# Optimization experiments

Hardware: AMD Instinct MI355X
Metric: run time of the kernel (lower is better)

## Reference

```python
import jax, jax.numpy as jnp
import numpy as np

B, T, N, H, E, K, HOR, OD = 64, 12, 1024, 64, 16, 3, 12, 1
DIN = 1  # input_dim
EPS = 1e-12


def setup_inputs() -> dict:
    key = jax.random.key(0)
    ks = jax.random.split(key, 8)
    s = 0.02
    return {
        "source": jax.random.normal(ks[0], (B, T, N, DIN), jnp.float32),
        "node_emb": jax.random.normal(ks[1], (N, E), jnp.float32),
        "time_emb": jax.random.normal(ks[2], (T, E), jnp.float32),
        "gate_wp": jax.random.normal(ks[3], (E, K, DIN + H, 2 * H), jnp.float32) * s,
        "gate_bp": jax.random.normal(ks[4], (E, 2 * H), jnp.float32) * s,
        "gate_lng": jnp.ones((E,), jnp.float32),
        "gate_lnb": jnp.zeros((E,), jnp.float32),
        "upd_wp": jax.random.normal(ks[5], (E, K, DIN + H, H), jnp.float32) * s,
        "upd_bp": jax.random.normal(ks[6], (E, H), jnp.float32) * s,
        "upd_lng": jnp.ones((E,), jnp.float32),
        "upd_lnb": jnp.zeros((E,), jnp.float32),
        "out_lng": jnp.ones((H,), jnp.float32),
        "out_lnb": jnp.zeros((H,), jnp.float32),
        "conv_w": jax.random.normal(ks[7], (HOR * OD, H), jnp.float32) * s,
        "conv_b": jnp.zeros((HOR * OD,), jnp.float32),
    }


def _ln(x, g, b):
    m = x.mean(-1, keepdims=True)
    v = x.var(-1, keepdims=True)
    return (x - m) / jnp.sqrt(v + EPS) * g + b


def _dagcn(x, node_emb, t_emb, wp, bp, lng, lnb):
    # x: [B, N, C]; node_emb: [N, E]; t_emb: [E] (one timestep)
    e = _ln(node_emb + t_emb[None, :], lng, lnb)          # [N, E] (dropout off in eval)
    sup = jax.nn.softmax(e @ e.T, axis=1)                  # [N, N]
    sl = [jnp.eye(N, dtype=x.dtype), sup]
    for _ in range(2, K):
        sl.append(2.0 * sup @ sl[-1] - sl[-2])             # Chebyshev recursion
    S = jnp.stack(sl, axis=0)                              # [K, N, N]
    w = jnp.einsum('nd,dkio->nkio', e, wp)                 # per-node weights
    bias = e @ bp                                          # [N, O]
    xg = jnp.einsum('knm,bmc->bnkc', S, x)                 # graph conv
    return jnp.einsum('bnki,nkio->bno', xg, w) + bias


def reference(source, node_emb, time_emb, gate_wp, gate_bp, gate_lng, gate_lnb,
              upd_wp, upd_bp, upd_lng, upd_lnb, out_lng, out_lnb, conv_w, conv_b):
    def step(state, xs):
        x_t, te = xs                                        # [B,N,DIN], [E]
        zr = jax.nn.sigmoid(_dagcn(jnp.concatenate([x_t, state], -1),
                                   node_emb, te, gate_wp, gate_bp, gate_lng, gate_lnb))
        z, r = zr[..., :H], zr[..., H:]
        hc = jnp.tanh(_dagcn(jnp.concatenate([x_t, z * state], -1),
                             node_emb, te, upd_wp, upd_bp, upd_lng, upd_lnb))
        h = r * state + (1.0 - r) * hc
        return h, None

    xs = jnp.swapaxes(source, 0, 1)                        # [T,B,N,DIN]
    h0 = jnp.zeros((B, N, H), source.dtype)
    h, _ = jax.lax.scan(step, h0, (xs, time_emb))          # last hidden state [B,N,H]
    y = _ln(h, out_lng, out_lnb)                           # out_dropout off in eval
    out = jnp.einsum('bnh,oh->bon', y, conv_w) + conv_b[None, :, None]  # end_conv
    return out.reshape(B, HOR, OD, N).transpose(0, 1, 3, 2)  # [B,horizon,N,output_dim]
```

## Files before the change

### kernel.cpp

```cpp
#include <hip/hip_runtime.h>
#include <math.h>

namespace {
constexpr int B_ = 64, T_ = 12, N_ = 1024, H_ = 64, E_ = 16;
constexpr int C_  = 65;
constexpr int BC_ = B_ * C_;
constexpr int NPAD_ = 4224;
constexpr int OG_ = 128;
constexpr int OU_ = 64;
constexpr float EPS_ = 1e-12f;
constexpr int KP_ = 224;
constexpr int KS_ = 232;
constexpr int COLG_ = OG_ * KP_;
constexpr int COLU_ = OU_ * KP_;
constexpr int NE_ = N_ * E_;
}

typedef unsigned short u16;
typedef unsigned int u32;
using f16x8 = __attribute__((ext_vector_type(8))) _Float16;
using f16x4 = __attribute__((ext_vector_type(4))) _Float16;
using f32x4 = __attribute__((ext_vector_type(4))) float;

__device__ __forceinline__ u32 div65(u32 x) { return (x * 16135u) >> 20; }
__device__ __forceinline__ u32 div29(u32 x) { return (x * 565u) >> 14; }

__device__ __forceinline__ void gl_lds16(const void* g, void* l, int lane) {
#if __has_builtin(__builtin_amdgcn_global_load_lds)
  __builtin_amdgcn_global_load_lds((const __attribute__((address_space(1))) u32*)g,
                                   (__attribute__((address_space(3))) u32*)l, 16, 0, 0);
#else
  *(uint4*)((char*)l + lane * 16) = *(const uint4*)g;
#endif
}

__device__ __forceinline__ void wprep_body(const float* __restrict__ wp, int NO,
                                           _Float16* __restrict__ wpC, int k, int tid) {
  if (tid >= NO) return;
  f16x8 lo = {}, hi = {};
  if (k < 195) {
    const u32 seg = div65((u32)k);
    const u32 ii = k - seg * 65;
#pragma unroll
    for (int d = 0; d < 8; d++)
      lo[d] = (_Float16)wp[(((size_t)d * 3 + seg) * 65 + ii) * NO + tid];
#pragma unroll
    for (int d = 0; d < 8; d++)
      hi[d] = (_Float16)wp[(((size_t)(d + 8) * 3 + seg) * 65 + ii) * NO + tid];
  }
  _Float16* dst = &wpC[((size_t)tid * KP_ + k) * 16];
  *(f16x8*)dst = lo;
  *(f16x8*)(dst + 8) = hi;
}

__device__ __forceinline__ void sup_body(const float* __restrict__ eT,
                                         _Float16* __restrict__ s16,
                                         int n, int tid, float* red) {
  float en[E_];
#pragma unroll
  for (int d = 0; d < E_; d++) en[d] = eT[d * N_ + n];
  float lg[4];
  float mx = -3.4e38f;
#pragma unroll
  for (int j = 0; j < 4; j++) {
    int m = tid + 256 * j;
    float s = 0.f;
#pragma unroll
    for (int d = 0; d < E_; d++) s = fmaf(en[d], eT[d * N_ + m], s);
    lg[j] = s;
    mx = fmaxf(mx, s);
  }
  red[tid] = mx; __syncthreads();
  for (int off = 128; off > 0; off >>= 1) {
    if (tid < off) red[tid] = fmaxf(red[tid], red[tid + off]);
    __syncthreads();
  }
  mx = red[0]; __syncthreads();
  float sum = 0.f;
#pragma unroll
  for (int j = 0; j < 4; j++) { lg[j] = __expf(lg[j] - mx); sum += lg[j]; }
  red[tid] = sum; __syncthreads();
  for (int off = 128; off > 0; off >>= 1) {
    if (tid < off) red[tid] += red[tid + off];
    __syncthreads();
  }
  float inv = 1.0f / red[0];
#pragma unroll
  for (int j = 0; j < 4; j++)
    s16[(size_t)n * N_ + tid + 256 * j] = (_Float16)(lg[j] * inv);
}

__device__ __forceinline__ void wgen_body(const float* __restrict__ e,
                                          const _Float16* __restrict__ wpC, int COLS,
                                          _Float16* __restrict__ Wt,
                                          int xb, int yb, int tid, float (*es)[16]) {
  const int col0 = xb * 1024 + tid * 4;
  const int n0 = yb * 64;
#pragma unroll
  for (int q = 0; q < 4; q++) {
    int idx = tid + q * 256;
    es[idx >> 4][idx & 15] = e[(size_t)n0 * 16 + idx];
  }
  __syncthreads();
  float wc[4][16];
#pragma unroll
  for (int cc = 0; cc < 4; cc++) {
    f16x8 a = *(const f16x8*)&wpC[(size_t)(col0 + cc) * 16];
    f16x8 b = *(const f16x8*)&wpC[(size_t)(col0 + cc) * 16 + 8];
#pragma unroll
    for (int d = 0; d < 8; d++) { wc[cc][d] = (float)a[d]; wc[cc][8 + d] = (float)b[d]; }
  }
  for (int nn = 0; nn < 64; nn++) {
    float acc[4] = {};
#pragma unroll
    for (int d = 0; d < 16; d++) {
      float ev = es[nn][d];
#pragma unroll
      for (int cc = 0; cc < 4; cc++) acc[cc] = fmaf(ev, wc[cc][d], acc[cc]);
    }
    f16x4 pv;
#pragma unroll
    for (int cc = 0; cc < 4; cc++) pv[cc] = (_Float16)acc[cc];
    *(f16x4*)&Wt[(size_t)(n0 + nn) * COLS + col0] = pv;
  }
}

__device__ __forceinline__ void supT_body(const _Float16* __restrict__ S,
                                          _Float16* __restrict__ ST,
                                          int tile, int tid, _Float16 (*lds)[66]) {
  const int n0 = (tile >> 4) * 64;
  const int m0 = (tile & 15) * 64;
  {
    const int r = tid >> 2, c0 = (tid & 3) * 16;
    const _Float16* sp = &S[(size_t)(n0 + r) * 1024 + m0 + c0];
    f16x8 a = *(const f16x8*)sp;
    f16x8 b = *(const f16x8*)(sp + 8);
#pragma unroll
    for (int i = 0; i < 8; i++) { lds[r][c0 + i] = a[i]; lds[r][c0 + 8 + i] = b[i]; }
  }
  __syncthreads();
  {
    const int c = tid >> 2, r0 = (tid & 3) * 16;
    f16x8 a, b;
#pragma unroll
    for (int i = 0; i < 8; i++) { a[i] = lds[r0 + i][c]; b[i] = lds[r0 + 8 + i][c]; }
    _Float16* dp = &ST[(size_t)(m0 + c) * 1024 + n0 + r0];
    *(f16x8*)dp = a;
    *(f16x8*)(dp + 8) = b;
  }
}

__device__ __forceinline__ void gemm_body(
    const _Float16* __restrict__ A, const _Float16* __restrict__ Bt,
    _Float16* __restrict__ rowout,
    int bx, int by, int tid, _Float16* As, _Float16* Bs) {
  const int wave = tid >> 6, lane = tid & 63;
  const int m0 = by * 128, c0 = bx * 64;
  const int lrow = lane >> 3;
  const int lchunk = lane & 7;
  const int fm = lane & 15, fq = lane >> 4;
  f32x4 acc[2][4] = {};
  for (int ks = 0; ks < 16; ks++) {
    const int kp = ks * 64;
#pragma unroll
    for (int q = 0; q < 4; q++) {
      const int seg = wave * 4 + q;
      const int row = seg * 8 + lrow;
      const int sw = lchunk ^ (row & 7);
      gl_lds16(A + (size_t)(m0 + row) * 1024 + kp + sw * 8, &As[seg * 8 * 64], lane);
    }
#pragma unroll
    for (int q = 0; q < 2; q++) {
      const int seg = wave * 2 + q;
      const int row = seg * 8 + lrow;
      const int sw = lchunk ^ (row & 7);
      gl_lds16(Bt + (size_t)(c0 + row) * 1024 + kp + sw * 8, &Bs[seg * 8 * 64], lane);
    }
    __syncthreads();
#pragma unroll
    for (int kk = 0; kk < 2; kk++) {
      f16x8 af[2], bfr[4];
      const int g = kk * 4 + fq;
#pragma unroll
      for (int mt = 0; mt < 2; mt++) {
        const int row = wave * 32 + mt * 16 + fm;
        af[mt] = *(const f16x8*)&As[row * 64 + (g ^ (row & 7)) * 8];
      }
#pragma unroll
      for (int nt = 0; nt < 4; nt++) {
        const int row = nt * 16 + fm;
        bfr[nt] = *(const f16x8*)&Bs[row * 64 + (g ^ (row & 7)) * 8];
      }
#pragma unroll
      for (int mt = 0; mt < 2; mt++)
#pragma unroll
        for (int nt = 0; nt < 4; nt++)
          acc[mt][nt] = __builtin_amdgcn_mfma_f32_16x16x32_f16(af[mt], bfr[nt], acc[mt][nt], 0, 0, 0);
    }
    __syncthreads();
  }
  const int q4 = fq * 4;
#pragma unroll
  for (int nt = 0; nt < 4; nt++) {
    const int col = c0 + nt * 16 + fm;
#pragma unroll
    for (int mt = 0; mt < 2; mt++) {
      const int row = m0 + wave * 32 + mt * 16 + q4;
      const f32x4 v = acc[mt][nt];
#pragma unroll
      for (int j = 0; j < 4; j++)
        rowout[(size_t)(row + j) * 1024 + col] = (_Float16)v[j];
    }
  }
}

__device__ __forceinline__ void gemm2_body(
    const _Float16* __restrict__ A1, const _Float16* __restrict__ A2,
    const _Float16* __restrict__ Bt,
    _Float16* __restrict__ y1row, _Float16* __restrict__ y2row,
    int bx, int by, int tid,
    _Float16* As1, _Float16* As2, _Float16* Bs) {
  const int wave = tid >> 6, lane = tid & 63;
  const int m0 = by * 128, c0 = bx * 64;
  const int lrow = lane >> 3;
  const int lchunk = lane & 7;
  const int fm = lane & 15, fq = lane >> 4;
  f32x4 acc1[2][4] = {}, acc2[2][4] = {};
  for (int ks = 0; ks < 16; ks++) {
    const int kp = ks * 64;
#pragma unroll
    for (int q = 0; q < 4; q++) {
      const int seg = wave * 4 + q;
      const int row = seg * 8 + lrow;
      const int sw = lchunk ^ (row & 7);
      const size_t go = (size_t)(m0 + row) * 1024 + kp + sw * 8;
      gl_lds16(A1 + go, &As1[seg * 8 * 64], lane);
      gl_lds16(A2 + go, &As2[seg * 8 * 64], lane);
    }
#pragma unroll
    for (int q = 0; q < 2; q++) {
      const int seg = wave * 2 + q;
      const int row = seg * 8 + lrow;
      const int sw = lchunk ^ (row & 7);
      gl_lds16(Bt + (size_t)(c0 + row) * 1024 + kp + sw * 8, &Bs[seg * 8 * 64], lane);
    }
    __syncthreads();
#pragma unroll
    for (int kk = 0; kk < 2; kk++) {
      f16x8 a1[2], a2[2], bfr[4];
      const int g = kk * 4 + fq;
#pragma unroll
      for (int mt = 0; mt < 2; mt++) {
        const int row = wave * 32 + mt * 16 + fm;
        const int o = row * 64 + (g ^ (row & 7)) * 8;
        a1[mt] = *(const f16x8*)&As1[o];
        a2[mt] = *(const f16x8*)&As2[o];
      }
#pragma unroll
      for (int nt = 0; nt < 4; nt++) {
        const int row = nt * 16 + fm;
        bfr[nt] = *(const f16x8*)&Bs[row * 64 + (g ^ (row & 7)) * 8];
      }
#pragma unroll
      for (int mt = 0; mt < 2; mt++)
#pragma unroll
        for (int nt = 0; nt < 4; nt++) {
          acc1[mt][nt] = __builtin_amdgcn_mfma_f32_16x16x32_f16(a1[mt], bfr[nt], acc1[mt][nt], 0, 0, 0);
          acc2[mt][nt] = __builtin_amdgcn_mfma_f32_16x16x32_f16(a2[mt], bfr[nt], acc2[mt][nt], 0, 0, 0);
        }
    }
    __syncthreads();
  }
  const int q4 = fq * 4;
#pragma unroll
  for (int nt = 0; nt < 4; nt++) {
    const int col = c0 + nt * 16 + fm;
    if (col >= BC_) continue;
#pragma unroll
    for (int mt = 0; mt < 2; mt++) {
      const int row = m0 + wave * 32 + mt * 16 + q4;
      const f32x4 v1 = acc1[mt][nt];
      const f32x4 v2 = acc2[mt][nt];
#pragma unroll
      for (int j = 0; j < 4; j++) {
        y1row[(size_t)(row + j) * BC_ + col] = (_Float16)v1[j];
        y2row[(size_t)(row + j) * BC_ + col] = (_Float16)v2[j];
      }
    }
  }
}

__device__ __forceinline__ void stage_xg(
    const _Float16* __restrict__ x0p, const _Float16* __restrict__ y1p,
    const _Float16* __restrict__ y2p, int tid, _Float16* __restrict__ XGs) {
  for (int idx = tid; idx < BC_; idx += 256) {
    const u32 b = div65((u32)idx), k = (u32)idx - b * 65;
    XGs[b * KS_ + k] = x0p[idx];
  }
  for (int idx = tid; idx < BC_; idx += 256) {
    const u32 b = div65((u32)idx), k = (u32)idx - b * 65;
    XGs[b * KS_ + 65 + k] = y1p[idx];
  }
  for (int idx = tid; idx < BC_; idx += 256) {
    const u32 b = div65((u32)idx), k = (u32)idx - b * 65;
    XGs[b * KS_ + 130 + k] = (_Float16)(2.f * (float)y2p[idx] - (float)x0p[idx]);
  }
  for (int idx = tid; idx < 64 * 29; idx += 256) {
    const u32 b = div29((u32)idx), k = (u32)idx - b * 29;
    XGs[b * KS_ + 195 + k] = (_Float16)0.f;
  }
}

__global__ __launch_bounds__(256) void k_pre0(
    const float* __restrict__ gate_wp, const float* __restrict__ upd_wp,
    _Float16* __restrict__ wpCg, _Float16* __restrict__ wpCu,
    const float* __restrict__ node_emb, const float* __restrict__ time_emb,
    const float* __restrict__ g_lng, const float* __restrict__ g_lnb,
    const float* __restrict__ u_lng, const float* __restrict__ u_lnb,
    float* __restrict__ eg_all, float* __restrict__ egT_all,
    float* __restrict__ eu_all, float* __restrict__ euT_all) {
  const int bid = blockIdx.x, tid = threadIdx.x;
  if (bid < KP_)     { wprep_body(gate_wp, OG_, wpCg, bid, tid); return; }
  if (bid < 2 * KP_) { wprep_body(upd_wp,  OU_, wpCu, bid - KP_, tid); return; }
  const int idx = bid - 2 * KP_;
  const int t = idx >> 2;
  const int n = (idx & 3) * 256 + tid;
  float v[E_];
  float m = 0.f;
#pragma unroll
  for (int d = 0; d < E_; d++) { v[d] = node_emb[n * E_ + d] + time_emb[t * E_ + d]; m += v[d]; }
  m *= (1.0f / E_);
  float var = 0.f;
#pragma unroll
  for (int d = 0; d < E_; d++) { float x = v[d] - m; var += x * x; }
  var *= (1.0f / E_);
  float rs = rsqrtf(var + EPS_);
#pragma unroll
  for (int d = 0; d < E_; d++) {
    float nv = (v[d] - m) * rs;
    float g = nv * g_lng[d] + g_lnb[d];
    float u = nv * u_lng[d] + u_lnb[d];
    eg_all[(size_t)t * NE_ + n * E_ + d] = g;
    egT_all[(size_t)t * NE_ + d * N_ + n] = g;
    eu_all[(size_t)t * NE_ + n * E_ + d] = u;
    euT_all[(size_t)t * NE_ + d * N_ + n] = u;
  }
}

__global__ __launch_bounds__(256) void k_pro(
    const float* __restrict__ egT0, const float* __restrict__ euT0,
    const float* __restrict__ src,
    _Float16* __restrict__ supG, _Float16* __restrict__ supU0,
    _Float16* __restrict__ Xt, _Float16* __restrict__ X0row) {
  __shared__ float red[256];
  const int bid = blockIdx.x, tid = threadIdx.x;
  if (bid < 1024) { sup_body(egT0, supG, bid, tid, red); return; }
  if (bid < 2048) { sup_body(euT0, supU0, bid - 1024, tid, red); return; }
  const int idx = bid - 2048;
  const int b = idx & 63, m0 = (idx >> 6) * 64;
  for (int q = 0; q < 17; q++) {
    int i = tid + q * 256;
    if (i < 64 * 65) {
      int c = i >> 6, m = i & 63;
      float xv = (c == 0) ? src[((size_t)b * T_) * N_ + m0 + m] : 0.f;
      Xt[((size_t)(b * C_ + c)) * 1024 + m0 + m] = (_Float16)xv;
      u32 mm = div65((u32)i), cc = (u32)i - mm * 65;
      float xv2 = (cc == 0) ? src[((size_t)b * T_) * N_ + m0 + mm] : 0.f;
      X0row[((size_t)(m0 + mm)) * BC_ + b * 65 + cc] = (_Float16)xv2;
    }
  }
}

__global__ __launch_bounds__(256) void k_proT(
    const _Float16* __restrict__ supG0, const _Float16* __restrict__ supU0,
    _Float16* __restrict__ supGT, _Float16* __restrict__ supUT) {
  __shared__ _Float16 lds[64][66];
  const int bid = blockIdx.x;
  if (bid < 256) supT_body(supG0, supGT, bid, threadIdx.x, lds);
  else           supT_body(supU0, supUT, bid - 256, threadIdx.x, lds);
}

__global__ __launch_bounds__(256) void k_pro2(
    const _Float16* __restrict__ supG0, const _Float16* __restrict__ supGT,
    const _Float16* __restrict__ supU0, const _Float16* __restrict__ supUT,
    _Float16* __restrict__ sup2G0, _Float16* __restrict__ sup2U0) {
  __shared__ __align__(16) _Float16 smem[12288];
  const int bid = blockIdx.x, tid = threadIdx.x;
  if (bid < 128)
    gemm_body(supG0, supGT, sup2G0, bid % 16, bid / 16, tid, smem, smem + 8192);
  else
    gemm_body(supU0, supUT, sup2U0, (bid - 128) % 16, (bid - 128) / 16, tid, smem, smem + 8192);
}

__global__ __launch_bounds__(256) void k_tr(const _Float16* __restrict__ X0,
                                            _Float16* __restrict__ Xt) {
  __shared__ _Float16 tile[64][66];
  const int c0 = (blockIdx.x % 65) * 64;
  const int m0 = (blockIdx.x / 65) * 64;
  const int tid = threadIdx.x;
#pragma unroll
  for (int q = 0; q < 16; q++) {
    int idx = tid + q * 256;
    int m = idx >> 6, c = idx & 63;
    tile[m][c] = X0[(size_t)(m0 + m) * BC_ + c0 + c];
  }
  __syncthreads();
  {
    const int c = tid >> 2, mq = (tid & 3) * 16;
    f16x8 a, b;
#pragma unroll
    for (int i = 0; i < 8; i++) { a[i] = tile[mq + i][c]; b[i] = tile[mq + 8 + i][c]; }
    _Float16* dp = &Xt[(size_t)(c0 + c) * 1024 + m0 + mq];
    *(f16x8*)dp = a;
    *(f16x8*)(dp + 8) = b;
  }
}

__global__ __launch_bounds__(256) void k_ga(
    const _Float16* __restrict__ supG_t, const _Float16* __restrict__ sup2G_t,
    const _Float16* __restrict__ Xt,
    _Float16* __restrict__ y1row, _Float16* __restrict__ y2row,
    const float* __restrict__ eg_t, const _Float16* __restrict__ wpCg,
    _Float16* __restrict__ WtG,
    const float* __restrict__ egT_nx, const float* __restrict__ euT_nx,
    _Float16* __restrict__ supG_nx, _Float16* __restrict__ supU_nx) {
  __shared__ __align__(16) _Float16 smem[20480];
  const int bid = blockIdx.x, tid = threadIdx.x;
  if (bid < 528) {
    gemm2_body(supG_t, sup2G_t, Xt, y1row, y2row, bid % 66, bid / 66, tid,
               smem, smem + 8192, smem + 16384);
  } else if (bid < 976) {
    const int w = bid - 528;
    wgen_body(eg_t, wpCg, COLG_, WtG, w % 28, w / 28, tid, (float(*)[16])smem);
  } else if (bid < 2000) {
    sup_body(egT_nx, supG_nx, bid - 976, tid, (float*)smem);
  } else {
    sup_body(euT_nx, supU_nx, bid - 2000, tid, (float*)smem);
  }
}

__global__ __launch_bounds__(256) void k_cgT(
    const float* __restrict__ eg,
    const _Float16* __restrict__ X0, const _Float16* __restrict__ y1r,
    const _Float16* __restrict__ y2r,
    const _Float16* __restrict__ Wt, const float* __restrict__ bp,
    const _Float16* __restrict__ h16, const float* __restrict__ src, int t,
    _Float16* __restrict__ r16, _Float16* X0out,
    const _Float16* __restrict__ supG_nx, const _Float16* __restrict__ supU_nx,
    _Float16* __restrict__ supGT, _Float16* __restrict__ supUT) {
  __shared__ __align__(16) char smraw[30272];
  const int bid = blockIdx.x;
  const int tid = threadIdx.x;
  if (bid >= 1024) {
    _Float16 (*lds)[66] = (_Float16(*)[66])smraw;
    if (bid < 1280) supT_body(supG_nx, supGT, bid - 1024, tid, lds);
    else            supT_body(supU_nx, supUT, bid - 1280, tid, lds);
    return;
  }
  float* es = (float*)smraw;
  float* bias_s = (float*)(smraw + 64);
  _Float16* XGs = (_Float16*)(smraw + 576);
  _Float16 (*zs)[72] = (_Float16(*)[72])(smraw + 576);
  _Float16 (*rs)[72] = (_Float16(*)[72])(smraw + 9792);
  const int n = bid;
  const int wave = tid >> 6, lane = tid & 63;
  const int fm = lane & 15, fq = lane >> 4;
  const int wm = wave >> 1, wn = wave & 1;
  if (tid < 16) es[tid] = eg[n * 16 + tid];
  stage_xg(X0 + (size_t)n * BC_, y1r + (size_t)n * BC_, y2r + (size_t)n * BC_, tid, XGs);
  __syncthreads();
  if (tid < 128) {
    float bv = 0.f;
#pragma unroll
    for (int d = 0; d < 16; d++) bv = fmaf(es[d], bp[d * OG_ + tid], bv);
    bias_s[tid] = bv;
  }
  const _Float16* Bb = Wt + (size_t)n * OG_ * KP_;
  f32x4 acc[2][4] = {};
#pragma unroll
  for (int kk = 0; kk < 7; kk++) {
    const int ko = kk * 32 + fq * 8;
    f16x8 af[2], bf[4];
#pragma unroll
    for (int mt = 0; mt < 2; mt++)
      af[mt] = *(const f16x8*)&XGs[(wm * 32 + mt * 16 + fm) * KS_ + ko];
#pragma unroll
    for (int nt = 0; nt < 4; nt++)
      bf[nt] = *(const f16x8*)&Bb[(wn * 64 + nt * 16 + fm) * KP_ + ko];
#pragma unroll
    for (int mt = 0; mt < 2; mt++)
#pragma unroll
      for (int nt = 0; nt < 4; nt++)
        acc[mt][nt] = __builtin_amdgcn_mfma_f32_16x16x32_f16(af[mt], bf[nt], acc[mt][nt], 0, 0, 0);
  }
  __syncthreads();
#pragma unroll
  for (int nt = 0; nt < 4; nt++) {
    const int o = wn * 64 + nt * 16 + fm;
    const float bias = bias_s[o];
#pragma unroll
    for (int mt = 0; mt < 2; mt++) {
      const f32x4 v = acc[mt][nt];
#pragma unroll
      for (int j = 0; j < 4; j++) {
        const int b = wm * 32 + mt * 16 + fq * 4 + j;
        float s = 1.0f / (1.0f + __expf(-(v[j] + bias)));
        if (wn == 0) zs[b][o] = (_Float16)s;
        else         rs[b][o - H_] = (_Float16)s;
      }
    }
  }
  __syncthreads();
  {
    const int b = tid >> 2, q = tid & 3;
    const _Float16* hp = &h16[((size_t)b * N_ + n) * H_ + q * 16];
    _Float16* xp = &X0out[(size_t)n * BC_ + b * 65 + 1 + q * 16];
    _Float16* rp = &r16[((size_t)b * N_ + n) * H_ + q * 16];
    f16x8 r0, r1;
#pragma unroll
    for (int i = 0; i < 8; i++) {
      r0[i] = rs[b][q * 16 + i];
      r1[i] = rs[b][q * 16 + 8 + i];
    }
    *(f16x8*)rp = r0;
    *(f16x8*)(rp + 8) = r1;
    f16x8 h0 = *(const f16x8*)hp;
    f16x8 h1 = *(const f16x8*)(hp + 8);
    f16x8 x0, x1;
#pragma unroll
    for (int i = 0; i < 8; i++) {
      x0[i] = (_Float16)((float)zs[b][q * 16 + i] * (float)h0[i]);
      x1[i] = (_Float16)((float)zs[b][q * 16 + 8 + i] * (float)h1[i]);
    }
    *(f16x8*)xp = x0;
    *(f16x8*)(xp + 8) = x1;
    if (tid < 64) {
      float sv = src[((size_t)tid * T_ + t) * N_ + n];
      X0out[(size_t)n * BC_ + tid * 65] = (_Float16)sv;
    }
  }
}

__global__ __launch_bounds__(256) void k_gu(
    const _Float16* __restrict__ supU_t, const _Float16* __restrict__ sup2U_t,
    const _Float16* __restrict__ Xt,
    _Float16* __restrict__ y1row, _Float16* __restrict__ y2row,
    const float* __restrict__ eu_t, const _Float16* __restrict__ wpCu,
    _Float16* __restrict__ WtU,
    const _Float16* __restrict__ supG_nx, const _Float16* __restrict__ supGT,
    const _Float16* __restrict__ supU_nx, const _Float16* __restrict__ supUT,
    _Float16* __restrict__ sup2G_nx, _Float16* __restrict__ sup2U_nx) {
  __shared__ __align__(16) _Float16 smem[20480];
  const int bid = blockIdx.x, tid = threadIdx.x;
  if (bid < 528) {
    gemm2_body(supU_t, sup2U_t, Xt, y1row, y2row, bid % 66, bid / 66, tid,
               smem, smem + 8192, smem + 16384);
  } else if (bid < 752) {
    const int w = bid - 528;
    wgen_body(eu_t, wpCu, COLU_, WtU, w % 14, w / 14, tid, (float(*)[16])smem);
  } else if (bid < 880) {
    const int w = bid - 752;
    gemm_body(supG_nx, supGT, sup2G_nx, w % 16, w / 16, tid, smem, smem + 8192);
  } else {
    const int w = bid - 880;
    gemm_body(supU_nx, supUT, sup2U_nx, w % 16, w / 16, tid, smem, smem + 8192);
  }
}

__global__ __launch_bounds__(256) void k_cu(
    const float* __restrict__ eu,
    const _Float16* __restrict__ X0, const _Float16* __restrict__ y1r,
    const _Float16* __restrict__ y2r,
    const _Float16* __restrict__ Wt, const float* __restrict__ bp,
    const _Float16* __restrict__ r16, const float* __restrict__ src,
    int t, int donext,
    _Float16* __restrict__ h16, _Float16* X0out) {
  __shared__ __align__(16) char smraw[30016];
  float* es = (float*)smraw;
  float* bias_s = (float*)(smraw + 64);
  _Float16* XGs = (_Float16*)(smraw + 320);
  _Float16 (*hs)[72] = (_Float16(*)[72])(smraw + 320);
  _Float16 (*rs)[72] = (_Float16(*)[72])(smraw + 9536);
  const int n = blockIdx.x;
  const int tid = threadIdx.x;
  const int wave = tid >> 6, lane = tid & 63;
  const int fm = lane & 15, fq = lane >> 4;
  if (tid < 16) es[tid] = eu[n * 16 + tid];
  stage_xg(X0 + (size_t)n * BC_, y1r + (size_t)n * BC_, y2r + (size_t)n * BC_, tid, XGs);
  __syncthreads();
  if (tid < 64) {
    float bv = 0.f;
#pragma unroll
    for (int d = 0; d < 16; d++) bv = fmaf(es[d], bp[d * OU_ + tid], bv);
    bias_s[tid] = bv;
  }
  const _Float16* Bb = Wt + (size_t)n * OU_ * KP_;
  f32x4 acc[4] = {};
#pragma unroll
  for (int kk = 0; kk < 7; kk++) {
    const int ko = kk * 32 + fq * 8;
    f16x8 af = *(const f16x8*)&XGs[(wave * 16 + fm) * KS_ + ko];
    f16x8 bf[4];
#pragma unroll
    for (int nt = 0; nt < 4; nt++)
      bf[nt] = *(const f16x8*)&Bb[(nt * 16 + fm) * KP_ + ko];
#pragma unroll
    for (int nt = 0; nt < 4; nt++)
      acc[nt] = __builtin_amdgcn_mfma_f32_16x16x32_f16(af, bf[nt], acc[nt], 0, 0, 0);
  }
  __syncthreads();
  {
    const int b = tid >> 2, q = tid & 3;
    const _Float16* hp = &h16[((size_t)b * N_ + n) * H_ + q * 16];
    const _Float16* rp = &r16[((size_t)b * N_ + n) * H_ + q * 16];
    f16x8 h0 = *(const f16x8*)hp;
    f16x8 h1 = *(const f16x8*)(hp + 8);
    f16x8 r0 = *(const f16x8*)rp;
    f16x8 r1 = *(const f16x8*)(rp + 8);
#pragma unroll
    for (int i = 0; i < 8; i++) {
      hs[b][q * 16 + i] = h0[i];
      hs[b][q * 16 + 8 + i] = h1[i];
      rs[b][q * 16 + i] = r0[i];
      rs[b][q * 16 + 8 + i] = r1[i];
    }
  }
  __syncthreads();
#pragma unroll
  for (int nt = 0; nt < 4; nt++) {
    const int o = nt * 16 + fm;
    const float bias = bias_s[o];
    const f32x4 v = acc[nt];
#pragma unroll
    for (int j = 0; j < 4; j++) {
      const int b = wave * 16 + fq * 4 + j;
      float hc = tanhf(v[j] + bias);
      float rv = (float)rs[b][o];
      float hv = (float)hs[b][o];
      hs[b][o] = (_Float16)(rv * hv + (1.0f - rv) * hc);
    }
  }
  __syncthreads();
  {
    const int b = tid >> 2, q = tid & 3;
    _Float16* hp = &h16[((size_t)b * N_ + n) * H_ + q * 16];
    f16x8 h0, h1;
#pragma unroll
    for (int i = 0; i < 8; i++) {
      h0[i] = hs[b][q * 16 + i];
      h1[i] = hs[b][q * 16 + 8 + i];
    }
    *(f16x8*)hp = h0;
    *(f16x8*)(hp + 8) = h1;
    if (donext) {
      _Float16* xp = &X0out[(size_t)n * BC_ + b * 65 + 1 + q * 16];
      *(f16x8*)xp = h0;
      *(f16x8*)(xp + 8) = h1;
      if (tid < 64) {
        float sv = src[((size_t)tid * T_ + (t + 1)) * N_ + n];
        X0out[(size_t)n * BC_ + tid * 65] = (_Float16)sv;
      }
    }
  }
}

__global__ __launch_bounds__(256) void k_final(const _Float16* __restrict__ h16,
                                               const float* __restrict__ out_lng,
                                               const float* __restrict__ out_lnb,
                                               const float* __restrict__ conv_w,
                                               const float* __restrict__ conv_b,
                                               float* __restrict__ out) {
  const int b = blockIdx.x >> 2;
  const int n = (blockIdx.x & 3) * 256 + threadIdx.x;
  __shared__ float cw[12][64];
  __shared__ float cb[12];
  __shared__ float lgs[64], lbs[64];
  for (int idx = threadIdx.x; idx < 12 * 64; idx += 256) cw[idx >> 6][idx & 63] = conv_w[idx];
  if (threadIdx.x < 12) cb[threadIdx.x] = conv_b[threadIdx.x];
  if (threadIdx.x < 64) { lgs[threadIdx.x] = out_lng[threadIdx.x]; lbs[threadIdx.x] = out_lnb[threadIdx.x]; }
  __syncthreads();
  const _Float16* hp = &h16[((size_t)b * N_ + n) * H_];
  float hv[64];
  float mean = 0.f;
#pragma unroll
  for (int i8 = 0; i8 < 8; i8++) {
    f16x8 v = *(const f16x8*)&hp[i8 * 8];
#pragma unroll
    for (int j = 0; j < 8; j++) { hv[i8 * 8 + j] = (float)v[j]; mean += hv[i8 * 8 + j]; }
  }
  mean *= (1.0f / H_);
  float var = 0.f;
#pragma unroll
  for (int i = 0; i < 64; i++) { float d = hv[i] - mean; var += d * d; }
  var *= (1.0f / H_);
  const float rs = rsqrtf(var + EPS_);
  float y[64];
#pragma unroll
  for (int i = 0; i < 64; i++)
    y[i] = (hv[i] - mean) * rs * lgs[i] + lbs[i];
#pragma unroll
  for (int o = 0; o < 12; o++) {
    float acc = cb[o];
#pragma unroll
    for (int i = 0; i < 64; i++) acc = fmaf(y[i], cw[o][i], acc);
    out[((size_t)b * 12 + o) * N_ + n] = acc;
  }
}

extern "C" void kernel_launch(void* const* d_in, const int* in_sizes, int n_in,
                              void* d_out, int out_size, void* d_ws, size_t ws_size,
                              hipStream_t stream) {
  const float* src      = (const float*)d_in[0];
  const float* node_emb = (const float*)d_in[1];
  const float* time_emb = (const float*)d_in[2];
  const float* gate_wp  = (const float*)d_in[3];
  const float* gate_bp  = (const float*)d_in[4];
  const float* gate_lng = (const float*)d_in[5];
  const float* gate_lnb = (const float*)d_in[6];
  const float* upd_wp   = (const float*)d_in[7];
  const float* upd_bp   = (const float*)d_in[8];
  const float* upd_lng  = (const float*)d_in[9];
  const float* upd_lnb  = (const float*)d_in[10];
  const float* out_lng  = (const float*)d_in[11];
  const float* out_lnb  = (const float*)d_in[12];
  const float* conv_w   = (const float*)d_in[13];
  const float* conv_b   = (const float*)d_in[14];
  float* out = (float*)d_out;

  constexpr size_t SZ_H16 = (size_t)B_ * N_ * H_ / 2;
  constexpr size_t SZ_R   = SZ_H16;
  constexpr size_t SZ_T   = (size_t)NPAD_ * 1024 / 2;
  constexpr size_t SZ_ROW = (size_t)N_ * BC_ / 2;
  constexpr size_t SZ_WT  = (size_t)N_ * OG_ * KP_ / 2;
  constexpr size_t SZ_WCG = (size_t)COLG_ * 16 / 2;
  constexpr size_t SZ_WCU = (size_t)COLU_ * 16 / 2;
  constexpr size_t SZ_S   = (size_t)N_ * N_ / 2;

  float* ws = (float*)d_ws;
  size_t off = 0;
  float* h16F   = ws + off; off += SZ_H16;
  float* r16F   = ws + off; off += SZ_R;
  float* XtF    = ws + off; off += SZ_T;
  float* X0F    = ws + off; off += SZ_ROW;
  float* y1F    = ws + off; off += SZ_ROW;
  float* y2F    = ws + off; off += SZ_ROW;
  float* WtF    = ws + off; off += SZ_WT;
  float* wcgF   = ws + off; off += SZ_WCG;
  float* wcuF   = ws + off; off += SZ_WCU;
  float* supGF  = ws + off; off += 2 * SZ_S;
  float* supUF  = ws + off; off += 2 * SZ_S;
  float* supGTF = ws + off; off += SZ_S;
  float* supUTF = ws + off; off += SZ_S;
  float* s2GF   = ws + off; off += 2 * SZ_S;
  float* s2UF   = ws + off; off += 2 * SZ_S;
  float* eg_all  = ws + off; off += (size_t)T_ * NE_;
  float* egT_all = ws + off; off += (size_t)T_ * NE_;
  float* eu_all  = ws + off; off += (size_t)T_ * NE_;
  float* euT_all = ws + off; off += (size_t)T_ * NE_;
  if (ws_size < off * sizeof(float)) return;

  _Float16* h16   = (_Float16*)h16F;
  _Float16* r16   = (_Float16*)r16F;
  _Float16* Xt    = (_Float16*)XtF;
  _Float16* X0row = (_Float16*)X0F;
  _Float16* y1row = (_Float16*)y1F;
  _Float16* y2row = (_Float16*)y2F;
  _Float16* WtG   = (_Float16*)WtF;
  _Float16* WtU   = (_Float16*)WtF;
  _Float16* wpCg  = (_Float16*)wcgF;
  _Float16* wpCu  = (_Float16*)wcuF;
  _Float16* supG  = (_Float16*)supGF;
  _Float16* supU  = (_Float16*)supUF;
  _Float16* supGT = (_Float16*)supGTF;
  _Float16* supUT = (_Float16*)supUTF;
  _Float16* s2G   = (_Float16*)s2GF;
  _Float16* s2U   = (_Float16*)s2UF;
  const size_t SB = (size_t)N_ * N_;

  hipMemsetAsync(h16, 0, SZ_H16 * sizeof(float), stream);
  k_pre0<<<2 * KP_ + 48, 256, 0, stream>>>(gate_wp, upd_wp, wpCg, wpCu,
                                           node_emb, time_emb,
                                           gate_lng, gate_lnb, upd_lng, upd_lnb,
                                           eg_all, egT_all, eu_all, euT_all);
  k_pro<<<3072, 256, 0, stream>>>(egT_all, euT_all, src, supG, supU, Xt, X0row);
  k_proT<<<512, 256, 0, stream>>>(supG, supU, supGT, supUT);
  k_pro2<<<256, 256, 0, stream>>>(supG, supGT, supU, supUT, s2G, s2U);

  for (int t = 0; t < T_; t++) {
    const int cur = t & 1, nxt = (t + 1) & 1;
    _Float16* supG_t  = supG + (size_t)cur * SB;
    _Float16* supG_nx = supG + (size_t)nxt * SB;
    _Float16* supU_t  = supU + (size_t)cur * SB;
    _Float16* supU_nx = supU + (size_t)nxt * SB;
    _Float16* s2G_t   = s2G + (size_t)cur * SB;
    _Float16* s2G_nx  = s2G + (size_t)nxt * SB;
    _Float16* s2U_t   = s2U + (size_t)cur * SB;
    _Float16* s2U_nx  = s2U + (size_t)nxt * SB;
    const float* eg_t = eg_all + (size_t)t * NE_;
    const float* eu_t = eu_all + (size_t)t * NE_;
    const int more = (t < T_ - 1) ? 1 : 0;
    const int tn = more ? t + 1 : t;

    k_ga<<<more ? 3024 : 976, 256, 0, stream>>>(
        supG_t, s2G_t, Xt, y1row, y2row, eg_t, wpCg, WtG,
        egT_all + (size_t)tn * NE_, euT_all + (size_t)tn * NE_, supG_nx, supU_nx);
    k_cgT<<<more ? 1536 : 1024, 256, 0, stream>>>(
        eg_t, X0row, y1row, y2row, WtG, gate_bp, h16, src, t, r16, X0row,
        supG_nx, supU_nx, supGT, supUT);
    k_tr<<<1040, 256, 0, stream>>>(X0row, Xt);
    k_gu<<<more ? 1008 : 752, 256, 0, stream>>>(
        supU_t, s2U_t, Xt, y1row, y2row, eu_t, wpCu, WtU,
        supG_nx, supGT, supU_nx, supUT, s2G_nx, s2U_nx);
    k_cu<<<N_, 256, 0, stream>>>(eu_t, X0row, y1row, y2row, WtU, upd_bp, r16,
                                 src, t, more, h16, X0row);
    if (more) k_tr<<<1040, 256, 0, stream>>>(X0row, Xt);
  }
  k_final<<<B_ * N_ / 256, 256, 0, stream>>>(h16, out_lng, out_lnb, conv_w, conv_b, out);
}
```

Before: 1.880 ms.

## Precompute all timestep supports and Chebyshev squares upfront in batched kernels

Moves the per-timestep support softmax, transpose and sup@sup GEMM out of the recurrent loop. They are now computed for all 12 timesteps in a few large batched launches before the scan, and the in-loop kernels carry only their own work. This trades fine-grained overlap of next-step support work with current-step kernels for large, well-filled launches and smaller in-loop grids. It costs much more workspace memory: 24 support matrices, 24 squared matrices and 12 transpose buffers.

```diff
diff --git a/kernel.cpp b/kernel.cpp
--- a/kernel.cpp
+++ b/kernel.cpp
@@ -347,16 +347,26 @@
   }
 }
 
-__global__ __launch_bounds__(256) void k_pro(
-    const float* __restrict__ egT0, const float* __restrict__ euT0,
+__global__ __launch_bounds__(256) void k_supall(
+    const float* __restrict__ egT_all, const float* __restrict__ euT_all,
     const float* __restrict__ src,
-    _Float16* __restrict__ supG, _Float16* __restrict__ supU0,
+    _Float16* __restrict__ supA,
     _Float16* __restrict__ Xt, _Float16* __restrict__ X0row) {
   __shared__ float red[256];
   const int bid = blockIdx.x, tid = threadIdx.x;
-  if (bid < 1024) { sup_body(egT0, supG, bid, tid, red); return; }
-  if (bid < 2048) { sup_body(euT0, supU0, bid - 1024, tid, red); return; }
-  const int idx = bid - 2048;
+  const size_t SB = (size_t)N_ * N_;
+  if (bid < 12288) {
+    const int t = bid >> 10, n = bid & 1023;
+    sup_body(egT_all + (size_t)t * NE_, supA + (size_t)(2 * t) * SB, n, tid, red);
+    return;
+  }
+  if (bid < 24576) {
+    const int idx = bid - 12288;
+    const int t = idx >> 10, n = idx & 1023;
+    sup_body(euT_all + (size_t)t * NE_, supA + (size_t)(2 * t + 1) * SB, n, tid, red);
+    return;
+  }
+  const int idx = bid - 24576;
   const int b = idx & 63, m0 = (idx >> 6) * 64;
   for (int q = 0; q < 17; q++) {
     int i = tid + q * 256;
@@ -371,25 +381,26 @@
   }
 }
 
-__global__ __launch_bounds__(256) void k_proT(
-    const _Float16* __restrict__ supG0, const _Float16* __restrict__ supU0,
-    _Float16* __restrict__ supGT, _Float16* __restrict__ supUT) {
+__global__ __launch_bounds__(256) void k_supT_half(
+    const _Float16* __restrict__ supA, _Float16* __restrict__ supTb, int half) {
   __shared__ _Float16 lds[64][66];
-  const int bid = blockIdx.x;
-  if (bid < 256) supT_body(supG0, supGT, bid, threadIdx.x, lds);
-  else           supT_body(supU0, supUT, bid - 256, threadIdx.x, lds);
-}
-
-__global__ __launch_bounds__(256) void k_pro2(
-    const _Float16* __restrict__ supG0, const _Float16* __restrict__ supGT,
-    const _Float16* __restrict__ supU0, const _Float16* __restrict__ supUT,
-    _Float16* __restrict__ sup2G0, _Float16* __restrict__ sup2U0) {
+  const size_t SB = (size_t)N_ * N_;
+  const int tile = blockIdx.x & 255;
+  const int p = blockIdx.x >> 8;
+  const int s = 2 * (half * 6 + (p >> 1)) + (p & 1);
+  supT_body(supA + (size_t)s * SB, supTb + (size_t)p * SB, tile, threadIdx.x, lds);
+}
+
+__global__ __launch_bounds__(256) void k_sup2_half(
+    const _Float16* __restrict__ supA, const _Float16* __restrict__ supTb,
+    _Float16* __restrict__ sup2A, int half) {
   __shared__ __align__(16) _Float16 smem[12288];
-  const int bid = blockIdx.x, tid = threadIdx.x;
-  if (bid < 128)
-    gemm_body(supG0, supGT, sup2G0, bid % 16, bid / 16, tid, smem, smem + 8192);
-  else
-    gemm_body(supU0, supUT, sup2U0, (bid - 128) % 16, (bid - 128) / 16, tid, smem, smem + 8192);
+  const size_t SB = (size_t)N_ * N_;
+  const int tile = blockIdx.x & 127;
+  const int p = blockIdx.x >> 7;
+  const int s = 2 * (half * 6 + (p >> 1)) + (p & 1);
+  gemm_body(supA + (size_t)s * SB, supTb + (size_t)p * SB, sup2A + (size_t)s * SB,
+            tile % 16, tile / 16, threadIdx.x, smem, smem + 8192);
 }
 
 __global__ __launch_bounds__(256) void k_tr(const _Float16* __restrict__ X0,
@@ -421,48 +432,33 @@
     const _Float16* __restrict__ Xt,
     _Float16* __restrict__ y1row, _Float16* __restrict__ y2row,
     const float* __restrict__ eg_t, const _Float16* __restrict__ wpCg,
-    _Float16* __restrict__ WtG,
-    const float* __restrict__ egT_nx, const float* __restrict__ euT_nx,
-    _Float16* __restrict__ supG_nx, _Float16* __restrict__ supU_nx) {
+    _Float16* __restrict__ WtG) {
   __shared__ __align__(16) _Float16 smem[20480];
   const int bid = blockIdx.x, tid = threadIdx.x;
   if (bid < 528) {
     gemm2_body(supG_t, sup2G_t, Xt, y1row, y2row, bid % 66, bid / 66, tid,
                smem, smem + 8192, smem + 16384);
-  } else if (bid < 976) {
+  } else {
     const int w = bid - 528;
     wgen_body(eg_t, wpCg, COLG_, WtG, w % 28, w / 28, tid, (float(*)[16])smem);
-  } else if (bid < 2000) {
-    sup_body(egT_nx, supG_nx, bid - 976, tid, (float*)smem);
-  } else {
-    sup_body(euT_nx, supU_nx, bid - 2000, tid, (float*)smem);
-  }
-}
-
-__global__ __launch_bounds__(256) void k_cgT(
+  }
+}
+
+__global__ __launch_bounds__(256) void k_cg(
     const float* __restrict__ eg,
     const _Float16* __restrict__ X0, const _Float16* __restrict__ y1r,
     const _Float16* __restrict__ y2r,
     const _Float16* __restrict__ Wt, const float* __restrict__ bp,
     const _Float16* __restrict__ h16, const float* __restrict__ src, int t,
-    _Float16* __restrict__ r16, _Float16* X0out,
-    const _Float16* __restrict__ supG_nx, const _Float16* __restrict__ supU_nx,
-    _Float16* __restrict__ supGT, _Float16* __restrict__ supUT) {
+    _Float16* __restrict__ r16, _Float16* X0out) {
   __shared__ __align__(16) char smraw[30272];
-  const int bid = blockIdx.x;
-  const int tid = threadIdx.x;
-  if (bid >= 1024) {
-    _Float16 (*lds)[66] = (_Float16(*)[66])smraw;
-    if (bid < 1280) supT_body(supG_nx, supGT, bid - 1024, tid, lds);
-    else            supT_body(supU_nx, supUT, bid - 1280, tid, lds);
-    return;
-  }
   float* es = (float*)smraw;
   float* bias_s = (float*)(smraw + 64);
   _Float16* XGs = (_Float16*)(smraw + 576);
   _Float16 (*zs)[72] = (_Float16(*)[72])(smraw + 576);
   _Float16 (*rs)[72] = (_Float16(*)[72])(smraw + 9792);
-  const int n = bid;
+  const int n = blockIdx.x;
+  const int tid = threadIdx.x;
   const int wave = tid >> 6, lane = tid & 63;
   const int fm = lane & 15, fq = lane >> 4;
   const int wm = wave >> 1, wn = wave & 1;
@@ -546,24 +542,15 @@
     const _Float16* __restrict__ Xt,
     _Float16* __restrict__ y1row, _Float16* __restrict__ y2row,
     const float* __restrict__ eu_t, const _Float16* __restrict__ wpCu,
-    _Float16* __restrict__ WtU,
-    const _Float16* __restrict__ supG_nx, const _Float16* __restrict__ supGT,
-    const _Float16* __restrict__ supU_nx, const _Float16* __restrict__ supUT,
-    _Float16* __restrict__ sup2G_nx, _Float16* __restrict__ sup2U_nx) {
+    _Float16* __restrict__ WtU) {
   __shared__ __align__(16) _Float16 smem[20480];
   const int bid = blockIdx.x, tid = threadIdx.x;
   if (bid < 528) {
     gemm2_body(supU_t, sup2U_t, Xt, y1row, y2row, bid % 66, bid / 66, tid,
                smem, smem + 8192, smem + 16384);
-  } else if (bid < 752) {
+  } else {
     const int w = bid - 528;
     wgen_body(eu_t, wpCu, COLU_, WtU, w % 14, w / 14, tid, (float(*)[16])smem);
-  } else if (bid < 880) {
-    const int w = bid - 752;
-    gemm_body(supG_nx, supGT, sup2G_nx, w % 16, w / 16, tid, smem, smem + 8192);
-  } else {
-    const int w = bid - 880;
-    gemm_body(supU_nx, supUT, sup2U_nx, w % 16, w / 16, tid, smem, smem + 8192);
   }
 }
 
@@ -747,12 +734,9 @@
   float* WtF    = ws + off; off += SZ_WT;
   float* wcgF   = ws + off; off += SZ_WCG;
   float* wcuF   = ws + off; off += SZ_WCU;
-  float* supGF  = ws + off; off += 2 * SZ_S;
-  float* supUF  = ws + off; off += 2 * SZ_S;
-  float* supGTF = ws + off; off += SZ_S;
-  float* supUTF = ws + off; off += SZ_S;
-  float* s2GF   = ws + off; off += 2 * SZ_S;
-  float* s2UF   = ws + off; off += 2 * SZ_S;
+  float* supAF  = ws + off; off += 24 * SZ_S;
+  float* sup2AF = ws + off; off += 24 * SZ_S;
+  float* supTbF = ws + off; off += 12 * SZ_S;
   float* eg_all  = ws + off; off += (size_t)T_ * NE_;
   float* egT_all = ws + off; off += (size_t)T_ * NE_;
   float* eu_all  = ws + off; off += (size_t)T_ * NE_;
@@ -769,12 +753,9 @@
   _Float16* WtU   = (_Float16*)WtF;
   _Float16* wpCg  = (_Float16*)wcgF;
   _Float16* wpCu  = (_Float16*)wcuF;
-  _Float16* supG  = (_Float16*)supGF;
-  _Float16* supU  = (_Float16*)supUF;
-  _Float16* supGT = (_Float16*)supGTF;
-  _Float16* supUT = (_Float16*)supUTF;
-  _Float16* s2G   = (_Float16*)s2GF;
-  _Float16* s2U   = (_Float16*)s2UF;
+  _Float16* supA  = (_Float16*)supAF;
+  _Float16* sup2A = (_Float16*)sup2AF;
+  _Float16* supTb = (_Float16*)supTbF;
   const size_t SB = (size_t)N_ * N_;
 
   hipMemsetAsync(h16, 0, SZ_H16 * sizeof(float), stream);
@@ -782,35 +763,26 @@
                                            node_emb, time_emb,
                                            gate_lng, gate_lnb, upd_lng, upd_lnb,
                                            eg_all, egT_all, eu_all, euT_all);
-  k_pro<<<3072, 256, 0, stream>>>(egT_all, euT_all, src, supG, supU, Xt, X0row);
-  k_proT<<<512, 256, 0, stream>>>(supG, supU, supGT, supUT);
-  k_pro2<<<256, 256, 0, stream>>>(supG, supGT, supU, supUT, s2G, s2U);
+  k_supall<<<25600, 256, 0, stream>>>(egT_all, euT_all, src, supA, Xt, X0row);
+  k_supT_half<<<3072, 256, 0, stream>>>(supA, supTb, 0);
+  k_sup2_half<<<1536, 256, 0, stream>>>(supA, supTb, sup2A, 0);
+  k_supT_half<<<3072, 256, 0, stream>>>(supA, supTb, 1);
+  k_sup2_half<<<1536, 256, 0, stream>>>(supA, supTb, sup2A, 1);
 
   for (int t = 0; t < T_; t++) {
-    const int cur = t & 1, nxt = (t + 1) & 1;
-    _Float16* supG_t  = supG + (size_t)cur * SB;
-    _Float16* supG_nx = supG + (size_t)nxt * SB;
-    _Float16* supU_t  = supU + (size_t)cur * SB;
-    _Float16* supU_nx = supU + (size_t)nxt * SB;
-    _Float16* s2G_t   = s2G + (size_t)cur * SB;
-    _Float16* s2G_nx  = s2G + (size_t)nxt * SB;
-    _Float16* s2U_t   = s2U + (size_t)cur * SB;
-    _Float16* s2U_nx  = s2U + (size_t)nxt * SB;
+    _Float16* supG_t  = supA  + (size_t)(2 * t) * SB;
+    _Float16* supU_t  = supA  + (size_t)(2 * t + 1) * SB;
+    _Float16* s2G_t   = sup2A + (size_t)(2 * t) * SB;
+    _Float16* s2U_t   = sup2A + (size_t)(2 * t + 1) * SB;
     const float* eg_t = eg_all + (size_t)t * NE_;
     const float* eu_t = eu_all + (size_t)t * NE_;
     const int more = (t < T_ - 1) ? 1 : 0;
-    const int tn = more ? t + 1 : t;
-
-    k_ga<<<more ? 3024 : 976, 256, 0, stream>>>(
-        supG_t, s2G_t, Xt, y1row, y2row, eg_t, wpCg, WtG,
-        egT_all + (size_t)tn * NE_, euT_all + (size_t)tn * NE_, supG_nx, supU_nx);
-    k_cgT<<<more ? 1536 : 1024, 256, 0, stream>>>(
-        eg_t, X0row, y1row, y2row, WtG, gate_bp, h16, src, t, r16, X0row,
-        supG_nx, supU_nx, supGT, supUT);
+
+    k_ga<<<976, 256, 0, stream>>>(supG_t, s2G_t, Xt, y1row, y2row, eg_t, wpCg, WtG);
+    k_cg<<<N_, 256, 0, stream>>>(eg_t, X0row, y1row, y2row, WtG, gate_bp, h16,
+                                 src, t, r16, X0row);
     k_tr<<<1040, 256, 0, stream>>>(X0row, Xt);
-    k_gu<<<more ? 1008 : 752, 256, 0, stream>>>(
-        supU_t, s2U_t, Xt, y1row, y2row, eu_t, wpCu, WtU,
-        supG_nx, supGT, supU_nx, supUT, s2G_nx, s2U_nx);
+    k_gu<<<752, 256, 0, stream>>>(supU_t, s2U_t, Xt, y1row, y2row, eu_t, wpCu, WtU);
     k_cu<<<N_, 256, 0, stream>>>(eu_t, X0row, y1row, y2row, WtU, upd_bp, r16,
                                  src, t, more, h16, X0row);
     if (more) k_tr<<<1040, 256, 0, stream>>>(X0row, Xt);
```

Result: slower. 1.988 ms (+5.7%).
